# Kernel tuning notes

Measured on AMD Instinct MI355X. Metric: run time of the kernel, lower is better.

Reference implementation:

```python
import jax, jax.numpy as jnp
import numpy as np

B, T, C, H, N = 2, 1024, 2048, 32, 64  # C == H*N, head_size fixed at 64
LAYER, NLAYERS = 12, 24
EPS = 1e-5 * 64.0  # GroupNorm eps = 1e-5 * 8**2


def _structured_params():
    r01 = LAYER / (NLAYERS - 1)          # ratio_0_to_1
    r1a0 = 1.0 - LAYER / NLAYERS         # ratio_1_to_almost0
    ddd = np.arange(C, dtype=np.float64) / C
    n = np.arange(C, dtype=np.float64)
    p = {}
    p['maa_x'] = 1.0 - ddd ** r1a0
    p['maa_w'] = 1.0 - ddd ** r1a0
    p['maa_k'] = 1.0 - ddd ** r1a0
    p['maa_v'] = 1.0 - (ddd ** r1a0 + 0.3 * r01)
    p['maa_r'] = 1.0 - ddd ** (0.5 * r1a0)
    p['maa_g'] = 1.0 - ddd ** (0.5 * r1a0)
    p['time_decay'] = -6.0 + 5.0 * (n / (C - 1)) ** (0.7 + 1.3 * r01)
    zig = ((n + 1) % 3 - 1) * 0.1
    p['u'] = (r01 * (1.0 - n / (C - 1)) + zig).reshape(H, N)  # time_faaaa
    return {k: jnp.asarray(v, jnp.float32) for k, v in p.items()}


def setup_inputs():
    key = jax.random.key(0)
    ks = jax.random.split(key, 12)
    inp = {'x': jax.random.normal(ks[0], (B, T, C), jnp.float32)}
    inp.update(_structured_params())
    inp['maa_w1'] = jax.random.uniform(ks[1], (C, 5 * 32), jnp.float32, -1e-4, 1e-4)
    inp['maa_w2'] = jax.random.uniform(ks[2], (5, 32, C), jnp.float32, -1e-4, 1e-4)
    inp['td_w1'] = jax.random.uniform(ks[3], (C, 64), jnp.float32, -1e-4, 1e-4)
    inp['td_w2'] = jax.random.uniform(ks[4], (64, C), jnp.float32, -1e-4, 1e-4)
    for i, name in enumerate(['Wr', 'Wk', 'Wv', 'Wg', 'Wo']):
        inp[name] = jax.random.normal(ks[5 + i], (C, C), jnp.float32) * 0.02  # applied as x @ W
    inp['ln_g'] = jnp.ones((C,), jnp.float32)
    inp['ln_b'] = jnp.zeros((C,), jnp.float32)
    return inp


def _wkv6(r, k, v, w, u):
    # r,k,v,w: [B,T,C]; u: [H,N].  y_t = r_t . (u*k_t v_t^T + S_t); S_{t+1} = exp(-exp(w_t))*S_t + k_t v_t^T
    def heads(a):
        return a.reshape(B, T, H, N).transpose(1, 0, 2, 3)  # [T,B,H,N]
    r, k, v = heads(r), heads(k), heads(v)
    d = jnp.exp(-jnp.exp(heads(w)))  # data-dependent per-channel decay

    def step(S, inp):
        r_t, k_t, v_t, d_t = inp  # each [B,H,N]
        y = jnp.einsum('bhj,bhji->bhi', r_t, S) \
            + jnp.sum(r_t * u * k_t, axis=-1, keepdims=True) * v_t
        S = d_t[..., None] * S + k_t[..., None] * v_t[..., None, :]
        return S, y

    S0 = jnp.zeros((B, H, N, N), jnp.float32)
    _, y = jax.lax.scan(step, S0, (r, k, v, d))
    return y.transpose(1, 0, 2, 3).reshape(B, T, C)


def reference(x, maa_x, maa_w, maa_k, maa_v, maa_r, maa_g, time_decay, u,
              maa_w1, maa_w2, td_w1, td_w2, Wr, Wk, Wv, Wg, Wo, ln_g, ln_b):
    # token shift: ZeroPad2d((0,0,1,-1)) == shift right by one along T with zero at t=0
    xx = jnp.pad(x, ((0, 0), (1, 0), (0, 0)))[:, :-1] - x
    xxx = x + xx * maa_x
    m = jnp.tanh(xxx @ maa_w1).reshape(B, T, 5, 32)
    m = jnp.einsum('btfd,fdc->fbtc', m, maa_w2)  # [5,B,T,C]
    mw, mk, mv, mr, mg = m[0], m[1], m[2], m[3], m[4]
    xw = x + xx * (maa_w + mw)
    xk = x + xx * (maa_k + mk)
    xv = x + xx * (maa_v + mv)
    xr = x + xx * (maa_r + mr)
    xg = x + xx * (maa_g + mg)
    r = xr @ Wr
    k = xk @ Wk
    v = xv @ Wv
    g = jax.nn.silu(xg @ Wg)
    w = time_decay + jnp.tanh(xw @ td_w1) @ td_w2  # [B,T,C]

    y = _wkv6(r, k, v, w, u)

    # GroupNorm(H groups over C), applied per (b,t) row
    yh = y.reshape(B, T, H, N)
    mu = yh.mean(-1, keepdims=True)
    var = yh.var(-1, keepdims=True)
    yn = (yh - mu) * jax.lax.rsqrt(var + EPS)
    yn = yn * ln_g.reshape(H, N) + ln_b.reshape(H, N)
    y = yn.reshape(B, T, C)
    return (y * g) @ Wo
```

## Files before the change

### kernel.cpp

```cpp
#include <hip/hip_runtime.h>
#include <cstdint>
#include <cstddef>

#define B_  2
#define T_  1024
#define C_  2048
#define H_  32
#define BT_ (B_*T_)
static constexpr float EPS_GN = 1e-5f * 64.0f;

using short8 = __attribute__((ext_vector_type(8))) short;
using f32x4  = __attribute__((ext_vector_type(4))) float;
typedef unsigned short bfu16;

__device__ __forceinline__ bfu16 f2b(float f) {
  uint32_t x = __float_as_uint(f);
  uint32_t r = (x + 0x7FFFu + ((x >> 16) & 1u)) >> 16;
  return (bfu16)r;
}
__device__ __forceinline__ float b2f(bfu16 h) {
  return __uint_as_float(((uint32_t)h) << 16);
}

__device__ __forceinline__ void gload16(const bfu16* g, bfu16* l) {
  __builtin_amdgcn_global_load_lds((__attribute__((address_space(1))) void*)g,
                                   (__attribute__((address_space(3))) void*)l,
                                   16, 0, 0);
}

struct G256P {
  const bfu16* Bt; float* of;
  size_t bStr, oStr;
  int ldk, nkt, kSplit;
  const bfu16* aArr[4];
};

__global__ __launch_bounds__(512, 2)
void gemm256(G256P p)
{
  extern __shared__ __align__(16) bfu16 sm[];
  const int tid  = threadIdx.x;
  const int nwg = gridDim.x * gridDim.y * gridDim.z;
  int lin = blockIdx.x + gridDim.x * (blockIdx.y + gridDim.y * blockIdx.z);
  lin = (lin & 7) * (nwg >> 3) + (lin >> 3);
  const int bx = lin % gridDim.x;
  const int by = (lin / gridDim.x) % gridDim.y;
  const int z  = lin / (gridDim.x * gridDim.y);
  const int m0   = by * 256, n0 = bx * 256;
  const int lane = tid & 63;
  const int wv   = tid >> 6;
  const int wm   = wv >> 2, wn = wv & 3;
  const int ldk  = p.ldk;

  const bfu16* A;
  size_t koff;
  if (p.kSplit > 1) { A = p.aArr[0]; koff = (size_t)z * p.nkt * 64; }
  else              { A = p.aArr[z]; koff = 0; }
  const bfu16* Bt = p.Bt + (size_t)z * p.bStr;

  const int srow = tid >> 3;
  const int scol = (tid & 7) * 8;
  const int sswz = (srow & 7) << 3;
  const bfu16* gA = A  + (size_t)(m0 + srow) * ldk + koff + (scol ^ sswz);
  const bfu16* gB = Bt + (size_t)(n0 + srow) * ldk + koff + (scol ^ sswz);

  auto STAGE_A = [&](bfu16* dst, int kt) {
    const bfu16* g = gA + (size_t)kt * 64;
    bfu16* l = dst + srow * 64 + scol;
#pragma unroll
    for (int it = 0; it < 4; ++it)
      gload16(g + (size_t)it * 64 * ldk, l + it * 4096);
  };
  auto STAGE_B = [&](bfu16* dst, int kt) {
    const bfu16* g = gB + (size_t)kt * 64;
    bfu16* l = dst + srow * 64 + scol;
#pragma unroll
    for (int it = 0; it < 4; ++it)
      gload16(g + (size_t)it * 64 * ldk, l + it * 4096);
  };

  f32x4 acc[8][4];
  const f32x4 zero = {0.f, 0.f, 0.f, 0.f};
#pragma unroll
  for (int i = 0; i < 8; ++i)
#pragma unroll
    for (int j = 0; j < 4; ++j) acc[i][j] = zero;

  STAGE_A(sm, 0);
  STAGE_B(sm + 32768, 0);

  const int rswz = (lane & 7) << 3;

  for (int kt = 0; kt < p.nkt; ++kt) {
    bfu16* curA = sm + (kt & 1) * 16384;
    bfu16* curB = sm + 32768 + (kt & 1) * 16384;
    bfu16* nxtA = sm + ((kt & 1) ^ 1) * 16384;
    bfu16* nxtB = sm + 32768 + ((kt & 1) ^ 1) * 16384;
    const bool more = (kt + 1 < p.nkt);
    if (more) {
      STAGE_A(nxtA, kt + 1);
      asm volatile("s_waitcnt vmcnt(4)" ::: "memory");
    } else {
      asm volatile("s_waitcnt vmcnt(0)" ::: "memory");
    }
    __builtin_amdgcn_s_barrier();

#pragma unroll
    for (int ks = 0; ks < 2; ++ks) {
      if (ks == 1 && more) STAGE_B(nxtB, kt + 1);
      const int ko = (ks * 32 + (lane >> 4) * 8) ^ rswz;
      short8 a[8], b[4];
#pragma unroll
      for (int i = 0; i < 8; ++i)
        a[i] = *(const short8*)(curA + (wm * 128 + i * 16 + (lane & 15)) * 64 + ko);
#pragma unroll
      for (int j = 0; j < 4; ++j)
        b[j] = *(const short8*)(curB + (wn * 64 + j * 16 + (lane & 15)) * 64 + ko);
      __builtin_amdgcn_s_setprio(1);
#pragma unroll
      for (int i = 0; i < 8; ++i)
#pragma unroll
        for (int j = 0; j < 4; ++j)
          acc[i][j] = __builtin_amdgcn_mfma_f32_16x16x32_bf16(a[i], b[j], acc[i][j], 0, 0, 0);
      __builtin_amdgcn_s_setprio(0);
    }
    __builtin_amdgcn_s_barrier();
  }

  float* o = p.of + (size_t)z * p.oStr;
  const int cb = n0 + wn * 64 + (lane & 15);
  const int rb = m0 + wm * 128 + ((lane >> 4) << 2);
#pragma unroll
  for (int i = 0; i < 8; ++i)
#pragma unroll
    for (int j = 0; j < 4; ++j) {
      int col = cb + j * 16;
#pragma unroll
      for (int q = 0; q < 4; ++q)
        o[(size_t)(rb + i * 16 + q) * 2048 + col] = acc[i][j][q];
    }
}

struct GemmP {
  const bfu16* A; const bfu16* Bt;
  float* of; bfu16* ob;
  const bfu16* xh; const bfu16* xxh;
  int ldk, kIters, kChunk, ldo;
  size_t pStride, aStr, bStr, oStr;
  const float* vArr[5];
};

template<int MODE>
__global__ __launch_bounds__(256)
void gemm_k(GemmP p)
{
  __shared__ alignas(16) bfu16 As[128*64];
  __shared__ alignas(16) bfu16 Bs[128*64];
  const int tid  = threadIdx.x;
  const int z    = blockIdx.z;
  const int m0   = blockIdx.y * 128, n0 = blockIdx.x * 128;
  const int lane = tid & 63;
  const int wv   = tid >> 6;
  const int wr   = (wv >> 1) * 64, wc = (wv & 1) * 64;

  const bfu16* A  = p.A;
  const bfu16* Bt = p.Bt;
  size_t koff = 0;
  if constexpr (MODE == 7) { A += (size_t)z * p.aStr; Bt += (size_t)z * p.bStr; }
  if constexpr (MODE == 5) { koff = (size_t)z * p.kChunk; }

  f32x4 acc[4][4];
  const f32x4 zero = {0.f, 0.f, 0.f, 0.f};
#pragma unroll
  for (int i = 0; i < 4; ++i)
#pragma unroll
    for (int j = 0; j < 4; ++j) acc[i][j] = zero;

  const int srow = tid >> 3;
  const int scol = (tid & 7) * 8;
  const int ldk  = p.ldk;

  for (int kb = 0; kb < p.kIters; ++kb) {
    const bfu16* ga = A  + (size_t)m0 * ldk + koff + kb * 64;
    const bfu16* gb = Bt + (size_t)n0 * ldk + koff + kb * 64;
#pragma unroll
    for (int it = 0; it < 4; ++it) {
      int r = it * 32 + srow;
      gload16(ga + (size_t)r * ldk + scol, As + r * 64 + scol);
      gload16(gb + (size_t)r * ldk + scol, Bs + r * 64 + scol);
    }
    __syncthreads();
#pragma unroll
    for (int kk = 0; kk < 2; ++kk) {
      const int ko = kk * 32 + (lane >> 4) * 8;
      short8 a[4], b[4];
#pragma unroll
      for (int i = 0; i < 4; ++i)
        a[i] = *(const short8*)(As + (wr + i * 16 + (lane & 15)) * 64 + ko);
#pragma unroll
      for (int j = 0; j < 4; ++j)
        b[j] = *(const short8*)(Bs + (wc + j * 16 + (lane & 15)) * 64 + ko);
#pragma unroll
      for (int i = 0; i < 4; ++i)
#pragma unroll
        for (int j = 0; j < 4; ++j)
          acc[i][j] = __builtin_amdgcn_mfma_f32_16x16x32_bf16(a[i], b[j], acc[i][j], 0, 0, 0);
    }
    __syncthreads();
  }

  const int cb = n0 + wc + (lane & 15);
  const int rb = m0 + wr + ((lane >> 4) << 2);
#pragma unroll
  for (int i = 0; i < 4; ++i) {
#pragma unroll
    for (int j = 0; j < 4; ++j) {
      int col = cb + j * 16;
#pragma unroll
      for (int q = 0; q < 4; ++q) {
        int row = rb + i * 16 + q;
        float v = acc[i][j][q];
        if constexpr (MODE == 4) {
          p.of[(size_t)row * p.ldo + col] = -__expf(p.vArr[0][col] + v);
        } else if constexpr (MODE == 5) {
          p.of[(size_t)z * p.pStride + (size_t)row * p.ldo + col] = v;
        } else if constexpr (MODE == 7) {
          size_t idx = (size_t)row * C_ + col;
          (p.ob + (size_t)z * p.oStr)[idx] =
              f2b(b2f(p.xh[idx]) + b2f(p.xxh[idx]) * (p.vArr[z][col] + v));
        }
      }
    }
  }
}

template<int OUT, int NS>
__global__ __launch_bounds__(256)
void redk_tanh(const float* __restrict__ part, size_t pStr, int ldo, int ncols,
               bfu16* __restrict__ out)
{
  int id = blockIdx.x * 256 + threadIdx.x;
  int row = id / ncols, col = id % ncols;
  if (row >= BT_) return;
  float v = 0.f;
#pragma unroll
  for (int s = 0; s < NS; ++s) v += part[(size_t)s * pStr + (size_t)row * ldo + col];
  bfu16 tv = f2b(tanhf(v));
  if constexpr (OUT == 0)
    out[((size_t)(col >> 5) * BT_ + row) * 64 + (col & 31)] = tv;
  else
    out[(size_t)row * 64 + col] = tv;
}

__global__ __launch_bounds__(256)
void redk_sum4(const float* __restrict__ p0, float* __restrict__ out)
{
  size_t i = ((size_t)blockIdx.x * 256 + threadIdx.x) * 4;
  const size_t str = (size_t)2048 * 2048;
  float4 a = *(const float4*)(p0 + i);
  float4 b = *(const float4*)(p0 + str + i);
  float4 c = *(const float4*)(p0 + 2 * str + i);
  float4 d = *(const float4*)(p0 + 3 * str + i);
  a.x += b.x + c.x + d.x; a.y += b.y + c.y + d.y;
  a.z += b.z + c.z + d.z; a.w += b.w + c.w + d.w;
  *(float4*)(out + i) = a;
}

struct TrP { const float* src[5]; bfu16* dst; size_t dStr; int R, Cc, Rpad, ldd; };

__global__ __launch_bounds__(256)
void transpose_k(TrP p)
{
  __shared__ float tile[32][33];
  const float* src = p.src[blockIdx.z];
  bfu16* dst = p.dst + (size_t)blockIdx.z * p.dStr;
  const int tx = threadIdx.x & 31, ty = threadIdx.x >> 5;
  const int r0 = blockIdx.y * 32, c0 = blockIdx.x * 32;
#pragma unroll
  for (int i = 0; i < 4; ++i) {
    int r = r0 + ty + i * 8, c = c0 + tx;
    tile[ty + i * 8][tx] = (r < p.R && c < p.Cc) ? src[(size_t)r * p.Cc + c] : 0.f;
  }
  __syncthreads();
#pragma unroll
  for (int i = 0; i < 4; ++i) {
    int c = c0 + ty + i * 8, r = r0 + tx;
    if (c < p.Cc && r < p.Rpad) dst[(size_t)c * p.ldd + r] = f2b(tile[tx][ty + i * 8]);
  }
}

__global__ __launch_bounds__(256)
void prep_xx(const float* __restrict__ x, const float* __restrict__ maa_x,
             bfu16* __restrict__ xxh, bfu16* __restrict__ xxx,
             bfu16* __restrict__ xh)
{
  size_t i = ((size_t)blockIdx.x * 256 + threadIdx.x) * 4;
  int c  = (int)(i & (C_ - 1));
  int bt = (int)(i >> 11);
  int t  = bt & (T_ - 1);
  float4 xv = *(const float4*)(x + i);
  float4 xp = {0.f, 0.f, 0.f, 0.f};
  if (t > 0) xp = *(const float4*)(x + i - C_);
  float4 mx = *(const float4*)(maa_x + c);
  float dx = xp.x - xv.x, dy = xp.y - xv.y, dz = xp.z - xv.z, dw = xp.w - xv.w;
  uint2 w0;
  w0.x = (uint32_t)f2b(dx) | ((uint32_t)f2b(dy) << 16);
  w0.y = (uint32_t)f2b(dz) | ((uint32_t)f2b(dw) << 16);
  *(uint2*)(xxh + i) = w0;
  uint2 w1;
  w1.x = (uint32_t)f2b(xv.x + dx * mx.x) | ((uint32_t)f2b(xv.y + dy * mx.y) << 16);
  w1.y = (uint32_t)f2b(xv.z + dz * mx.z) | ((uint32_t)f2b(xv.w + dw * mx.w) << 16);
  *(uint2*)(xxx + i) = w1;
  uint2 w2;
  w2.x = (uint32_t)f2b(xv.x) | ((uint32_t)f2b(xv.y) << 16);
  w2.y = (uint32_t)f2b(xv.z) | ((uint32_t)f2b(xv.w) << 16);
  *(uint2*)(xh + i) = w2;
}

#define S32 68

__global__ __launch_bounds__(256)
void wkv_a32(const float* __restrict__ r, const float* __restrict__ k,
             const float* __restrict__ v, const float* __restrict__ w,
             const float* __restrict__ u, float* __restrict__ rp,
             float* __restrict__ y, float* __restrict__ U, float* __restrict__ G)
{
  __shared__ float rw[32 * S32];
  __shared__ float kk[32 * S32];
  __shared__ float vv[32 * S32];
  __shared__ float Ps[32 * S32];
  __shared__ float red[256];
  __shared__ float diag[32];
  __shared__ float Gl[64];

  const int blk = blockIdx.x;
  const int bh = blk >> 5, c = blk & 31;
  const int b = bh >> 5, h = bh & 31;
  const int tid = threadIdx.x;
  const size_t gbase = ((size_t)(b * T_ + c * 32)) * C_ + h * 64;

  {
    const int t = tid >> 3, q = tid & 7;
    const size_t g = gbase + (size_t)t * C_ + q * 8;
    const int l = t * S32 + q * 8;
    *(float4*)(rw + l)     = *(const float4*)(r + g);
    *(float4*)(rw + l + 4) = *(const float4*)(r + g + 4);
    *(float4*)(kk + l)     = *(const float4*)(k + g);
    *(float4*)(kk + l + 4) = *(const float4*)(k + g + 4);
    *(float4*)(vv + l)     = *(const float4*)(v + g);
    *(float4*)(vv + l + 4) = *(const float4*)(v + g + 4);
    *(float4*)(Ps + l)     = *(const float4*)(w + g);
    *(float4*)(Ps + l + 4) = *(const float4*)(w + g + 4);
  }
  __syncthreads();

  {
    const int seg = tid >> 6, j = tid & 63;
    float loc = 0.f;
#pragma unroll
    for (int tt = 0; tt < 8; ++tt) loc += Ps[(seg * 8 + tt) * S32 + j];
    red[seg * 64 + j] = loc;
  }
  __syncthreads();
  {
    const int seg = tid >> 6, j = tid & 63;
    float cs = 0.f;
    for (int s = 0; s < seg; ++s) cs += red[s * 64 + j];
    const float uj = u[h * 64 + j];
#pragma unroll
    for (int tt = 0; tt < 8; ++tt) {
      const int a = (seg * 8 + tt) * S32 + j;
      float lw = Ps[a];
      float rv = rw[a] * __expf(cs);
      rw[a] = rv;
      cs += lw;
      float kv = kk[a] * __expf(-cs);
      kk[a] = kv;
      Ps[a] = rv * kv * uj * __expf(lw);
    }
    if (seg == 3) {
      float Gj = __expf(cs);
      Gl[j] = Gj;
      G[((size_t)bh * 32 + c) * 64 + j] = Gj;
    }
  }
  __syncthreads();

  {
    const int t = tid & 31, q = tid >> 5;
    float s = 0.f;
#pragma unroll
    for (int jj = 0; jj < 8; ++jj) s += Ps[t * S32 + q * 8 + jj];
    red[q * 32 + t] = s;
  }
  __syncthreads();
  if (tid < 32) {
    float d = 0.f;
#pragma unroll
    for (int q = 0; q < 8; ++q) d += red[q * 32 + tid];
    diag[tid] = d;
  }
  __syncthreads();

  {
    const int tq = tid >> 4, sq = tid & 15;
    float a00 = 0.f, a01 = 0.f, a10 = 0.f, a11 = 0.f;
    if (sq <= tq) {
      for (int j = 0; j < 64; j += 4) {
        float4 r0 = *(const float4*)(rw + (2 * tq + 0) * S32 + j);
        float4 r1 = *(const float4*)(rw + (2 * tq + 1) * S32 + j);
        float4 k0 = *(const float4*)(kk + (2 * sq + 0) * S32 + j);
        float4 k1 = *(const float4*)(kk + (2 * sq + 1) * S32 + j);
        a00 += r0.x * k0.x + r0.y * k0.y + r0.z * k0.z + r0.w * k0.w;
        a01 += r0.x * k1.x + r0.y * k1.y + r0.z * k1.z + r0.w * k1.w;
        a10 += r1.x * k0.x + r1.y * k0.y + r1.z * k0.z + r1.w * k0.w;
        a11 += r1.x * k1.x + r1.y * k1.y + r1.z * k1.z + r1.w * k1.w;
      }
    }
    __syncthreads();
    if (sq <= tq) {
      const float av[2][2] = {{a00, a01}, {a10, a11}};
#pragma unroll
      for (int tt = 0; tt < 2; ++tt)
#pragma unroll
        for (int ss = 0; ss < 2; ++ss) {
          int t = 2 * tq + tt, s = 2 * sq + ss;
          Ps[t * S32 + s] = (s < t) ? av[tt][ss] : (s == t ? diag[t] : 0.f);
        }
    }
  }
  __syncthreads();

  {
    const int tq = tid >> 4, iq = tid & 15;
    float o0[4] = {0.f, 0.f, 0.f, 0.f}, o1[4] = {0.f, 0.f, 0.f, 0.f};
    const int tmax = 2 * tq + 1;
    for (int s = 0; s <= tmax; ++s) {
      float4 vx = *(const float4*)(vv + s * S32 + iq * 4);
      float p0 = Ps[(2 * tq + 0) * S32 + s];
      float p1 = Ps[(2 * tq + 1) * S32 + s];
      o0[0] += p0 * vx.x; o0[1] += p0 * vx.y; o0[2] += p0 * vx.z; o0[3] += p0 * vx.w;
      o1[0] += p1 * vx.x; o1[1] += p1 * vx.y; o1[2] += p1 * vx.z; o1[3] += p1 * vx.w;
    }
    float4 w0 = {o0[0], o0[1], o0[2], o0[3]};
    float4 w1 = {o1[0], o1[1], o1[2], o1[3]};
    *(float4*)(y + gbase + (size_t)(2 * tq + 0) * C_ + iq * 4) = w0;
    *(float4*)(y + gbase + (size_t)(2 * tq + 1) * C_ + iq * 4) = w1;
  }

  {
    const int jq = tid >> 4, iq = tid & 15;
    float ua[4][4] = {{0.f}};
    for (int s = 0; s < 32; ++s) {
      float4 kx = *(const float4*)(kk + s * S32 + jq * 4);
      float4 vx = *(const float4*)(vv + s * S32 + iq * 4);
      ua[0][0] += kx.x * vx.x; ua[0][1] += kx.x * vx.y; ua[0][2] += kx.x * vx.z; ua[0][3] += kx.x * vx.w;
      ua[1][0] += kx.y * vx.x; ua[1][1] += kx.y * vx.y; ua[1][2] += kx.y * vx.z; ua[1][3] += kx.y * vx.w;
      ua[2][0] += kx.z * vx.x; ua[2][1] += kx.z * vx.y; ua[2][2] += kx.z * vx.z; ua[2][3] += kx.z * vx.w;
      ua[3][0] += kx.w * vx.x; ua[3][1] += kx.w * vx.y; ua[3][2] += kx.w * vx.z; ua[3][3] += kx.w * vx.w;
    }
    const size_t ub = ((size_t)bh * 32 + c) * 4096;
#pragma unroll
    for (int jj = 0; jj < 4; ++jj) {
      float g = Gl[jq * 4 + jj];
      float4 uv = {ua[jj][0] * g, ua[jj][1] * g, ua[jj][2] * g, ua[jj][3] * g};
      *(float4*)(U + ub + (size_t)(jq * 4 + jj) * 64 + iq * 4) = uv;
    }
  }

  {
    const int t = tid >> 3, q = tid & 7;
    const size_t g = gbase + (size_t)t * C_ + q * 8;
    const int l = t * S32 + q * 8;
    *(float4*)(rp + g)     = *(const float4*)(rw + l);
    *(float4*)(rp + g + 4) = *(const float4*)(rw + l + 4);
  }
}

__global__ __launch_bounds__(256)
void wkv_b32(const float* __restrict__ U, const float* __restrict__ G,
             float* __restrict__ Sbuf)
{
  const int bh = blockIdx.x >> 2, jq = blockIdx.x & 3;
  const int tid = threadIdx.x;
  const int j = jq * 16 + (tid >> 4);
  const int i = (tid & 15) * 4;
  float4 S = {0.f, 0.f, 0.f, 0.f};
  for (int c = 0; c < 32; ++c) {
    const size_t cb = ((size_t)bh * 32 + c);
    float g = G[cb * 64 + j];
    const size_t idx = cb * 4096 + (size_t)j * 64 + i;
    *(float4*)(Sbuf + idx) = S;
    float4 uv = *(const float4*)(U + idx);
    S.x = g * S.x + uv.x; S.y = g * S.y + uv.y;
    S.z = g * S.z + uv.z; S.w = g * S.w + uv.w;
  }
}

__global__ __launch_bounds__(256)
void wkv_c32(const float* __restrict__ rp, const float* __restrict__ Sbuf,
             const float* __restrict__ y, const float* __restrict__ gpre,
             const float* __restrict__ lng, const float* __restrict__ lnb,
             bfu16* __restrict__ yg)
{
  __shared__ float Sl[64 * S32];
  __shared__ float rl[32 * S32];
  const int blk = blockIdx.x;
  const int bh = blk >> 5, c = blk & 31;
  const int b = bh >> 5, h = bh & 31;
  const int tid = threadIdx.x;
  const size_t gbase = ((size_t)(b * T_ + c * 32)) * C_ + h * 64;
  {
    const int j = tid >> 2, q = tid & 3;
    const size_t sb = ((size_t)bh * 32 + c) * 4096 + (size_t)j * 64 + q * 16;
    const int l = j * S32 + q * 16;
#pragma unroll
    for (int p = 0; p < 4; ++p)
      *(float4*)(Sl + l + p * 4) = *(const float4*)(Sbuf + sb + p * 4);
    const int t = tid >> 3, q8 = tid & 7;
    const size_t gr = gbase + (size_t)t * C_ + q8 * 8;
    const int lr = t * S32 + q8 * 8;
    *(float4*)(rl + lr)     = *(const float4*)(rp + gr);
    *(float4*)(rl + lr + 4) = *(const float4*)(rp + gr + 4);
  }
  __syncthreads();
  const int tq = tid >> 4, iq = tid & 15;
  float o0[4] = {0.f, 0.f, 0.f, 0.f}, o1[4] = {0.f, 0.f, 0.f, 0.f};
  for (int j = 0; j < 64; ++j) {
    float4 sv = *(const float4*)(Sl + j * S32 + iq * 4);
    float r0 = rl[(2 * tq + 0) * S32 + j];
    float r1 = rl[(2 * tq + 1) * S32 + j];
    o0[0] += r0 * sv.x; o0[1] += r0 * sv.y; o0[2] += r0 * sv.z; o0[3] += r0 * sv.w;
    o1[0] += r1 * sv.x; o1[1] += r1 * sv.y; o1[2] += r1 * sv.z; o1[3] += r1 * sv.w;
  }
#pragma unroll
  for (int rr = 0; rr < 2; ++rr) {
    float* o = rr ? o1 : o0;
    const size_t rowb = gbase + (size_t)(2 * tq + rr) * C_;
    float4 yi = *(const float4*)(y + rowb + iq * 4);
    float yv[4] = {yi.x + o[0], yi.y + o[1], yi.z + o[2], yi.w + o[3]};
    float s = yv[0] + yv[1] + yv[2] + yv[3];
    float sq = yv[0] * yv[0] + yv[1] * yv[1] + yv[2] * yv[2] + yv[3] * yv[3];
#pragma unroll
    for (int m = 1; m < 16; m <<= 1) {
      s  += __shfl_xor(s, m, 64);
      sq += __shfl_xor(sq, m, 64);
    }
    float mu  = s * (1.f / 64.f);
    float var = sq * (1.f / 64.f) - mu * mu;
    float rs  = rsqrtf(var + EPS_GN);
    float4 gp = *(const float4*)(gpre + rowb + iq * 4);
    const float gpv[4] = {gp.x, gp.y, gp.z, gp.w};
    uint32_t pk[2];
    ushort hw[4];
#pragma unroll
    for (int e = 0; e < 4; ++e) {
      int cidx = h * 64 + iq * 4 + e;
      float yn = (yv[e] - mu) * rs * lng[cidx] + lnb[cidx];
      float gs = gpv[e] / (1.f + __expf(-gpv[e]));
      hw[e] = f2b(yn * gs);
    }
    pk[0] = (uint32_t)hw[0] | ((uint32_t)hw[1] << 16);
    pk[1] = (uint32_t)hw[2] | ((uint32_t)hw[3] << 16);
    *(uint2*)(yg + rowb + iq * 4) = make_uint2(pk[0], pk[1]);
  }
}

extern "C" void kernel_launch(void* const* d_in, const int* in_sizes, int n_in,
                              void* d_out, int out_size, void* d_ws, size_t ws_size,
                              hipStream_t stream)
{
  const float* x      = (const float*)d_in[0];
  const float* maa_x  = (const float*)d_in[1];
  const float* maa_w  = (const float*)d_in[2];
  const float* maa_k  = (const float*)d_in[3];
  const float* maa_v  = (const float*)d_in[4];
  const float* maa_r  = (const float*)d_in[5];
  const float* maa_g  = (const float*)d_in[6];
  const float* tdec   = (const float*)d_in[7];
  const float* u      = (const float*)d_in[8];
  const float* maa_w1 = (const float*)d_in[9];
  const float* maa_w2 = (const float*)d_in[10];
  const float* td_w1  = (const float*)d_in[11];
  const float* td_w2  = (const float*)d_in[12];
  const float* lng = (const float*)d_in[18];
  const float* lnb = (const float*)d_in[19];
  float* out = (float*)d_out;

  char* wsp = (char*)d_ws;
  auto alloc = [&](size_t bytes) -> char* {
    char* p = wsp;
    wsp += (bytes + 255) & ~(size_t)255;
    return p;
  };

  bfu16* WT0 = (bfu16*)alloc((size_t)5 * 2048 * 2048 * 2);
  bfu16* w1T  = (bfu16*)alloc((size_t)256 * 2048 * 2);
  bfu16* tw1T = (bfu16*)alloc((size_t)128 * 2048 * 2);
  bfu16* tw2T = (bfu16*)alloc((size_t)2048 * 64 * 2);
  bfu16* w2T  = (bfu16*)alloc((size_t)5 * 2048 * 64 * 2);
  float* ybuf = (float*)alloc((size_t)BT_ * C_ * 4);
  bfu16* xxh  = (bfu16*)alloc((size_t)BT_ * C_ * 2);
  bfu16* xxx  = (bfu16*)alloc((size_t)BT_ * C_ * 2);
  bfu16* xh   = (bfu16*)alloc((size_t)BT_ * C_ * 2);
  bfu16* mtan = (bfu16*)alloc((size_t)5 * BT_ * 64 * 2);
  bfu16* xmix0 = (bfu16*)alloc((size_t)5 * BT_ * C_ * 2);
  float* rbuf = (float*)alloc((size_t)4 * BT_ * C_ * 4);
  float* kbuf = rbuf + (size_t)BT_ * C_;
  float* vbuf = kbuf + (size_t)BT_ * C_;
  float* gbuf = vbuf + (size_t)BT_ * C_;
  float* wbuf = (float*)alloc((size_t)BT_ * C_ * 4);
  bfu16* wtan = (bfu16*)alloc((size_t)BT_ * 64 * 2);
  float* Sbuf = (float*)alloc((size_t)64 * 32 * 4096 * 4);
  float* Gbuf = (float*)alloc((size_t)64 * 32 * 64 * 4);
  bfu16* ygb  = xxx;
  float* Ubuf = (float*)(xmix0 + (size_t)1 * BT_ * C_);
  float* part1 = rbuf;
  float* part3 = wbuf;
  float* partW = rbuf;

  hipMemsetAsync(mtan, 0, (size_t)5 * BT_ * 64 * 2, stream);

  dim3 tb(256);

  {
    TrP p{}; for (int i = 0; i < 5; ++i) p.src[i] = (const float*)d_in[13 + i];
    p.dst = WT0; p.dStr = (size_t)2048 * 2048; p.R = 2048; p.Cc = 2048; p.Rpad = 2048; p.ldd = 2048;
    transpose_k<<<dim3(64, 64, 5), tb, 0, stream>>>(p);
  }
  {
    TrP p{}; p.src[0] = maa_w1; p.dst = w1T; p.dStr = 0;
    p.R = 2048; p.Cc = 160; p.Rpad = 2048; p.ldd = 2048;
    transpose_k<<<dim3(5, 64, 1), tb, 0, stream>>>(p);
  }
  {
    TrP p{}; p.src[0] = td_w1; p.dst = tw1T; p.dStr = 0;
    p.R = 2048; p.Cc = 64; p.Rpad = 2048; p.ldd = 2048;
    transpose_k<<<dim3(2, 64, 1), tb, 0, stream>>>(p);
  }
  {
    TrP p{}; p.src[0] = td_w2; p.dst = tw2T; p.dStr = 0;
    p.R = 64; p.Cc = 2048; p.Rpad = 64; p.ldd = 64;
    transpose_k<<<dim3(64, 2, 1), tb, 0, stream>>>(p);
  }
  {
    TrP p{}; for (int f = 0; f < 5; ++f) p.src[f] = maa_w2 + (size_t)f * 32 * 2048;
    p.dst = w2T; p.dStr = (size_t)2048 * 64;
    p.R = 32; p.Cc = 2048; p.Rpad = 64; p.ldd = 64;
    transpose_k<<<dim3(64, 2, 5), tb, 0, stream>>>(p);
  }

  prep_xx<<<dim3((BT_ * C_ / 4) / 256), tb, 0, stream>>>(x, maa_x, xxh, xxx, xh);

  {
    GemmP p{}; p.A = xxx; p.Bt = w1T; p.ldk = 2048; p.kIters = 4; p.kChunk = 256;
    p.ldo = 256; p.pStride = (size_t)BT_ * 256; p.of = part1;
    gemm_k<5><<<dim3(2, 16, 8), tb, 0, stream>>>(p);
  }
  redk_tanh<0, 8><<<dim3(BT_ * 160 / 256), tb, 0, stream>>>(part1, (size_t)BT_ * 256, 256, 160, mtan);

  {
    GemmP p{}; p.A = mtan; p.Bt = w2T; p.ldk = 64; p.kIters = 1;
    p.aStr = (size_t)BT_ * 64; p.bStr = (size_t)2048 * 64; p.oStr = (size_t)BT_ * C_;
    p.ob = xmix0; p.xh = xh; p.xxh = xxh;
    p.vArr[0] = maa_w; p.vArr[1] = maa_k; p.vArr[2] = maa_v; p.vArr[3] = maa_r; p.vArr[4] = maa_g;
    gemm_k<7><<<dim3(16, 16, 5), tb, 0, stream>>>(p);
  }

  {
    G256P p{}; p.Bt = WT0; p.ldk = 2048; p.nkt = 32; p.kSplit = 1;
    p.bStr = (size_t)2048 * 2048; p.oStr = (size_t)BT_ * C_; p.of = rbuf;
    p.aArr[0] = xmix0 + (size_t)3 * BT_ * C_;
    p.aArr[1] = xmix0 + (size_t)1 * BT_ * C_;
    p.aArr[2] = xmix0 + (size_t)2 * BT_ * C_;
    p.aArr[3] = xmix0 + (size_t)4 * BT_ * C_;
    gemm256<<<dim3(8, 8, 4), dim3(512), 131072, stream>>>(p);
  }

  {
    GemmP p{}; p.A = xmix0; p.Bt = tw1T; p.ldk = 2048; p.kIters = 2; p.kChunk = 128;
    p.ldo = 128; p.pStride = (size_t)BT_ * 128; p.of = part3;
    gemm_k<5><<<dim3(1, 16, 16), tb, 0, stream>>>(p);
  }
  redk_tanh<1, 16><<<dim3(BT_ * 64 / 256), tb, 0, stream>>>(part3, (size_t)BT_ * 128, 128, 64, wtan);

  {
    GemmP p{}; p.A = wtan; p.Bt = tw2T; p.ldk = 64; p.kIters = 1;
    p.of = wbuf; p.ldo = 2048; p.vArr[0] = tdec;
    gemm_k<4><<<dim3(16, 16, 1), tb, 0, stream>>>(p);
  }

  wkv_a32<<<dim3(2048), tb, 0, stream>>>(rbuf, kbuf, vbuf, wbuf, u, rbuf, ybuf, Ubuf, Gbuf);
  wkv_b32<<<dim3(256),  tb, 0, stream>>>(Ubuf, Gbuf, Sbuf);
  wkv_c32<<<dim3(2048), tb, 0, stream>>>(rbuf, Sbuf, ybuf, gbuf, lng, lnb, ygb);

  {
    G256P p{}; p.Bt = WT0 + (size_t)4 * 2048 * 2048; p.ldk = 2048;
    p.nkt = 8; p.kSplit = 4;
    p.bStr = 0; p.oStr = (size_t)2048 * 2048; p.of = partW;
    p.aArr[0] = ygb;
    gemm256<<<dim3(8, 8, 4), dim3(512), 131072, stream>>>(p);
  }
  redk_sum4<<<dim3(4096), tb, 0, stream>>>(partW, out);
}
```

Before: 317.1 us.

## Add 8-phase ping-pong pipelined 256x256 GEMM for the r/k/v/g projections

Adds a new 256x256-tile bf16 MFMA GEMM kernel that splits each 64-wide K step into two 32-wide halves and four compute phases. Each phase issues the next half-tile's global-to-LDS loads, separated by barriers and s_setprio. The r/k/v/g projection launch now uses this kernel instead of the previous gemm256. The goal is to hide global-load latency behind MFMA work and keep LDS reads interleaved with compute. The cost is many more barriers per K step and tighter timing constraints on the staging buffers.

```diff
diff --git a/kernel.cpp b/kernel.cpp
--- a/kernel.cpp
+++ b/kernel.cpp
@@ -26,6 +26,152 @@
   __builtin_amdgcn_global_load_lds((__attribute__((address_space(1))) void*)g,
                                    (__attribute__((address_space(3))) void*)l,
                                    16, 0, 0);
+}
+
+struct G8P {
+  const bfu16* Bt; float* of;
+  size_t bStr, oStr;
+  int ldk, nkt, kSplit;
+  const bfu16* aArr[4];
+};
+
+__global__ __launch_bounds__(512, 2)
+void gemm8p(G8P p)
+{
+  extern __shared__ __align__(16) bfu16 sm[];
+  const int tid  = threadIdx.x;
+  const int nwg = gridDim.x * gridDim.y * gridDim.z;
+  int lin = blockIdx.x + gridDim.x * (blockIdx.y + gridDim.y * blockIdx.z);
+  lin = (lin & 7) * (nwg >> 3) + (lin >> 3);
+  const int bx = lin % gridDim.x;
+  const int by = (lin / gridDim.x) % gridDim.y;
+  const int z  = lin / (gridDim.x * gridDim.y);
+  const int m0   = by * 256, n0 = bx * 256;
+  const int lane = tid & 63;
+  const int wv   = tid >> 6;
+  const int wm   = wv >> 2, wn = wv & 3;
+  const int ldk  = p.ldk;
+  const int nkt  = p.nkt;
+
+  const bfu16* A;
+  size_t koff;
+  if (p.kSplit > 1) { A = p.aArr[0]; koff = (size_t)z * nkt * 64; }
+  else              { A = p.aArr[z]; koff = 0; }
+  const bfu16* Bt = p.Bt + (size_t)z * p.bStr;
+
+  const int sr = tid >> 2;
+  const int sc = (tid & 3) * 8;
+  const bfu16* gAs = A  + (size_t)(m0 + sr) * ldk + koff + sc;
+  const bfu16* gBs = Bt + (size_t)(n0 + sr) * ldk + koff + sc;
+
+  auto STAGE_A = [&](int t, int h) {
+    bfu16* l = sm + (((t & 1) * 2 + h) << 13) + tid * 8;
+    const bfu16* g = gAs + (size_t)t * 64 + h * 32;
+    gload16(g, l);
+    gload16(g + (size_t)128 * ldk, l + 4096);
+  };
+  auto STAGE_B = [&](int t, int h) {
+    bfu16* l = sm + 32768 + (((t & 1) * 2 + h) << 13) + tid * 8;
+    const bfu16* g = gBs + (size_t)t * 64 + h * 32;
+    gload16(g, l);
+    gload16(g + (size_t)128 * ldk, l + 4096);
+  };
+
+  f32x4 acc[8][4];
+  const f32x4 zero = {0.f, 0.f, 0.f, 0.f};
+#pragma unroll
+  for (int i = 0; i < 8; ++i)
+#pragma unroll
+    for (int j = 0; j < 4; ++j) acc[i][j] = zero;
+
+  const int fr  = lane & 15;
+  const int q8  = (lane >> 4) * 8;
+  const int aoff = (wm * 128 + fr) * 32 + q8;
+  const int boff = (wn * 64 + fr) * 32 + q8;
+
+  STAGE_A(0, 0); STAGE_B(0, 0);
+  STAGE_A(0, 1); STAGE_B(0, 1);
+  STAGE_A(1, 0); STAGE_B(1, 0);
+  asm volatile("s_waitcnt vmcnt(4)" ::: "memory");
+  __builtin_amdgcn_s_barrier();
+
+  for (int t = 0; t < nkt; ++t) {
+    const bfu16* Ah0 = sm + (((t & 1) * 2 + 0) << 13);
+    const bfu16* Ah1 = sm + (((t & 1) * 2 + 1) << 13);
+    const bfu16* Bh0 = sm + 32768 + (((t & 1) * 2 + 0) << 13);
+    const bfu16* Bh1 = sm + 32768 + (((t & 1) * 2 + 1) << 13);
+    short8 a[4], b[4];
+
+#pragma unroll
+    for (int j = 0; j < 4; ++j) b[j] = *(const short8*)(Bh0 + boff + j * 512);
+#pragma unroll
+    for (int i = 0; i < 4; ++i) a[i] = *(const short8*)(Ah0 + aoff + i * 512);
+    if (t + 1 < nkt) STAGE_A(t + 1, 1);
+    __builtin_amdgcn_s_barrier();
+    __builtin_amdgcn_s_setprio(1);
+#pragma unroll
+    for (int i = 0; i < 4; ++i)
+#pragma unroll
+      for (int j = 0; j < 4; ++j)
+        acc[i][j] = __builtin_amdgcn_mfma_f32_16x16x32_bf16(a[i], b[j], acc[i][j], 0, 0, 0);
+    __builtin_amdgcn_s_setprio(0);
+    __builtin_amdgcn_s_barrier();
+
+#pragma unroll
+    for (int i = 0; i < 4; ++i) a[i] = *(const short8*)(Ah0 + aoff + (4 + i) * 512);
+    if (t + 1 < nkt) STAGE_B(t + 1, 1);
+    __builtin_amdgcn_s_barrier();
+    __builtin_amdgcn_s_setprio(1);
+#pragma unroll
+    for (int i = 0; i < 4; ++i)
+#pragma unroll
+      for (int j = 0; j < 4; ++j)
+        acc[4 + i][j] = __builtin_amdgcn_mfma_f32_16x16x32_bf16(a[i], b[j], acc[4 + i][j], 0, 0, 0);
+    __builtin_amdgcn_s_setprio(0);
+    __builtin_amdgcn_s_barrier();
+
+#pragma unroll
+    for (int j = 0; j < 4; ++j) b[j] = *(const short8*)(Bh1 + boff + j * 512);
+#pragma unroll
+    for (int i = 0; i < 4; ++i) a[i] = *(const short8*)(Ah1 + aoff + i * 512);
+    if (t + 2 < nkt) STAGE_A(t + 2, 0);
+    __builtin_amdgcn_s_barrier();
+    __builtin_amdgcn_s_setprio(1);
+#pragma unroll
+    for (int i = 0; i < 4; ++i)
+#pragma unroll
+      for (int j = 0; j < 4; ++j)
+        acc[i][j] = __builtin_amdgcn_mfma_f32_16x16x32_bf16(a[i], b[j], acc[i][j], 0, 0, 0);
+    __builtin_amdgcn_s_setprio(0);
+    __builtin_amdgcn_s_barrier();
+
+#pragma unroll
+    for (int i = 0; i < 4; ++i) a[i] = *(const short8*)(Ah1 + aoff + (4 + i) * 512);
+    if (t + 2 < nkt) STAGE_B(t + 2, 0);
+    __builtin_amdgcn_s_barrier();
+    __builtin_amdgcn_s_setprio(1);
+#pragma unroll
+    for (int i = 0; i < 4; ++i)
+#pragma unroll
+      for (int j = 0; j < 4; ++j)
+        acc[4 + i][j] = __builtin_amdgcn_mfma_f32_16x16x32_bf16(a[i], b[j], acc[4 + i][j], 0, 0, 0);
+    __builtin_amdgcn_s_setprio(0);
+    asm volatile("s_waitcnt vmcnt(4)" ::: "memory");
+    __builtin_amdgcn_s_barrier();
+  }
+
+  float* o = p.of + (size_t)z * p.oStr;
+  const int cb = n0 + wn * 64 + (lane & 15);
+  const int rb = m0 + wm * 128 + ((lane >> 4) << 2);
+#pragma unroll
+  for (int i = 0; i < 8; ++i)
+#pragma unroll
+    for (int j = 0; j < 4; ++j) {
+      int col = cb + j * 16;
+#pragma unroll
+      for (int q = 0; q < 4; ++q)
+        o[(size_t)(rb + i * 16 + q) * 2048 + col] = acc[i][j][q];
+    }
 }
 
 struct G256P {
@@ -668,13 +814,13 @@
   }
 
   {
-    G256P p{}; p.Bt = WT0; p.ldk = 2048; p.nkt = 32; p.kSplit = 1;
+    G8P p{}; p.Bt = WT0; p.ldk = 2048; p.nkt = 32; p.kSplit = 1;
     p.bStr = (size_t)2048 * 2048; p.oStr = (size_t)BT_ * C_; p.of = rbuf;
     p.aArr[0] = xmix0 + (size_t)3 * BT_ * C_;
     p.aArr[1] = xmix0 + (size_t)1 * BT_ * C_;
     p.aArr[2] = xmix0 + (size_t)2 * BT_ * C_;
     p.aArr[3] = xmix0 + (size_t)4 * BT_ * C_;
-    gemm256<<<dim3(8, 8, 4), dim3(512), 131072, stream>>>(p);
+    gemm8p<<<dim3(8, 8, 4), dim3(512), 131072, stream>>>(p);
   }
 
   {
```

After: 325.2 us. +2.6%, slower.
